# Optimization experiments

Hardware: AMD Instinct MI355X
Metric: run time of the kernel (lower is better)

Reference implementation:

```python
import jax, jax.numpy as jnp
import numpy as np

B, C, H, W = 4, 256, 48, 48
NH = 8
HD = C // NH
SCALE = HD ** -0.5


def setup_inputs() -> dict:
    key = jax.random.key(0)
    ks = jax.random.split(key, 9)
    std = 1.0 / np.sqrt(C)
    return {
        "x": jax.random.normal(ks[0], (B, C, H, W), dtype=jnp.float32),
        "Wq": jax.random.normal(ks[1], (C, C), dtype=jnp.float32) * std,
        "bq": jax.random.normal(ks[2], (C,), dtype=jnp.float32) * std,
        "Wk": jax.random.normal(ks[3], (C, C), dtype=jnp.float32) * std,
        "bk": jax.random.normal(ks[4], (C,), dtype=jnp.float32) * std,
        "Wv": jax.random.normal(ks[5], (C, C), dtype=jnp.float32) * std,
        "bv": jax.random.normal(ks[6], (C,), dtype=jnp.float32) * std,
        "Wo": jax.random.normal(ks[7], (C, C), dtype=jnp.float32) * std,
        "bo": jax.random.normal(ks[8], (C,), dtype=jnp.float32) * std,
    }


def _proj(x, Wm, bm):
    # 1x1 conv == pointwise channel matmul; x: [B,C,H,W], Wm: [out,in]
    return jnp.einsum('bchw,oc->bohw', x, Wm) + bm[None, :, None, None]


def reference(x, Wq, bq, Wk, bk, Wv, bv, Wo, bo):
    b, c, h, w = x.shape
    s = h * w
    # [B,C,H,W] -> [B, NH, S, HD]
    def heads(t):
        return t.reshape(b, NH, HD, s).transpose(0, 1, 3, 2)
    q = heads(_proj(x, Wq, bq))
    k = heads(_proj(x, Wk, bk))
    v = heads(_proj(x, Wv, bv))
    attn = jax.nn.softmax(jnp.einsum('bhsd,bhtd->bhst', q, k) * SCALE, axis=-1)
    out = jnp.einsum('bhst,bhtd->bhsd', attn, v)
    out = out.transpose(0, 1, 3, 2).reshape(b, c, h, w)
    out = _proj(out, Wo, bo)
    return out + x
```

## Files before the change

### kernel.cpp

```cpp
#include <hip/hip_runtime.h>
#include <hip/hip_bf16.h>

#define BATCH 4
#define CCH   256
#define SS    2304
#define NHEAD 8
#define HD    32
#define SCALE_L2E (1.4426950408889634f * 0.17677669529663687f)

using bf16x8 = __attribute__((ext_vector_type(8))) short;
using v4s    = __attribute__((ext_vector_type(4))) short;
using v8s    = __attribute__((ext_vector_type(8))) short;
using f32x4  = __attribute__((ext_vector_type(4))) float;

static __device__ __forceinline__ unsigned short f2bf(float f) {
    union { float f; unsigned u; } a; a.f = f;
    unsigned r = a.u + 0x7fff + ((a.u >> 16) & 1);
    return (unsigned short)(r >> 16);
}
static __device__ __forceinline__ unsigned pk2(float a, float b) {
    return (unsigned)f2bf(a) | ((unsigned)f2bf(b) << 16);
}
static __device__ __forceinline__ v4s pack4(float a, float b, float c, float d) {
    float2 lo; lo.x = a; lo.y = b;
    float2 hi; hi.x = c; hi.y = d;
    union { __hip_bfloat162 h2[2]; v4s s; } u;
    u.h2[0] = __float22bfloat162_rn(lo);
    u.h2[1] = __float22bfloat162_rn(hi);
    return u.s;
}

__global__ __launch_bounds__(256) void prep(const float* __restrict__ Wq, const float* __restrict__ Wk,
                                            const float* __restrict__ Wv, const float* __restrict__ Wo,
                                            const float* __restrict__ x,
                                            unsigned short* __restrict__ wqkv, unsigned short* __restrict__ wo,
                                            unsigned short* __restrict__ xt) {
    __shared__ float T[64][65];
    const int tid = threadIdx.x;
    if (blockIdx.x < 1024) {
        const int idx = blockIdx.x * 256 + tid;
        if (idx < 768 * 256) {
            const int o = idx >> 8, c = idx & 255;
            const float v = (o < 256) ? Wq[idx] : (o < 512) ? Wk[(o - 256) * 256 + c] : Wv[(o - 512) * 256 + c];
            wqkv[idx] = f2bf(v);
        } else {
            const int j = idx - 768 * 256;
            wo[j] = f2bf(Wo[j]);
        }
    } else {
        const int e = blockIdx.x - 1024;
        const int b = e / 144, rem = e % 144;
        const int c0 = (rem / 36) * 64, s0 = (rem % 36) * 64;
        #pragma unroll
        for (int p = 0; p < 16; ++p) {
            const int c = p * 4 + (tid >> 6), s = tid & 63;
            T[c][s] = x[((size_t)(b * CCH + c0 + c)) * SS + s0 + s];
        }
        __syncthreads();
        #pragma unroll
        for (int p = 0; p < 8; ++p) {
            const int s = p * 8 + (tid >> 5), c = (tid & 31) * 2;
            *(unsigned*)&xt[((size_t)(b * SS + s0 + s)) * CCH + c0 + c] = pk2(T[c][s], T[c + 1][s]);
        }
    }
}

__global__ __launch_bounds__(128) void gemm_qkv(const unsigned short* __restrict__ xt,
                                                const unsigned short* __restrict__ wqkv,
                                                const float* __restrict__ bq, const float* __restrict__ bk,
                                                const float* __restrict__ bv,
                                                unsigned short* __restrict__ qt, unsigned short* __restrict__ kt,
                                                unsigned short* __restrict__ vp) {
    __shared__ char Eb[2][9216];
    const int b  = blockIdx.z;
    const int o0 = blockIdx.x * 64, s0 = blockIdx.y * 64;
    const int tid = threadIdx.x, wid = tid >> 6, lane = tid & 63;
    const int lr = lane & 15, lg = lane >> 4;
    const int o_w = o0 + wid * 32, s_w = s0;

    const f32x4 zero4 = {0.f, 0.f, 0.f, 0.f};
    f32x4 acc[2][4];
    #pragma unroll
    for (int ai = 0; ai < 2; ++ai)
        #pragma unroll
        for (int bj = 0; bj < 4; ++bj) acc[ai][bj] = zero4;

    #pragma unroll
    for (int c0 = 0; c0 < 256; c0 += 32) {
        bf16x8 a[2], bb[4];
        #pragma unroll
        for (int ai = 0; ai < 2; ++ai)
            a[ai] = *(const bf16x8*)&wqkv[(size_t)(o_w + ai * 16 + lr) * 256 + c0 + lg * 8];
        #pragma unroll
        for (int bj = 0; bj < 4; ++bj)
            bb[bj] = *(const bf16x8*)&xt[((size_t)b * SS + s_w + bj * 16 + lr) * 256 + c0 + lg * 8];
        #pragma unroll
        for (int ai = 0; ai < 2; ++ai)
            #pragma unroll
            for (int bj = 0; bj < 4; ++bj)
                acc[ai][bj] = __builtin_amdgcn_mfma_f32_16x16x32_bf16(a[ai], bb[bj], acc[ai][bj], 0, 0, 0);
    }

    const int t = o0 >> 8;
    const int o_loc = o_w - t * 256;
    const float* bias = (t == 0) ? bq : (t == 1) ? bk : bv;

    float vals[2][4][4];
    #pragma unroll
    for (int ai = 0; ai < 2; ++ai)
        #pragma unroll
        for (int bj = 0; bj < 4; ++bj)
            #pragma unroll
            for (int i = 0; i < 4; ++i) {
                float vv = acc[ai][bj][i] + bias[o_loc + ai * 16 + 4 * lg + i];
                if (t == 0) vv *= SCALE_L2E;
                vals[ai][bj][i] = vv;
            }

    if (t < 2) {
        unsigned short* dst = (t == 0) ? qt : kt;
        unsigned short* Ls = (unsigned short*)Eb[wid];
        #pragma unroll
        for (int ai = 0; ai < 2; ++ai)
            #pragma unroll
            for (int bj = 0; bj < 4; ++bj) {
                uint2 w;
                w.x = pk2(vals[ai][bj][0], vals[ai][bj][1]);
                w.y = pk2(vals[ai][bj][2], vals[ai][bj][3]);
                *(uint2*)&Ls[(bj * 16 + lr) * 40 + ai * 16 + 4 * lg] = w;
            }
        const int h = o_loc >> 5;
        const size_t base = (size_t)(b * NHEAD + h) * SS;
        #pragma unroll
        for (int p = 0; p < 4; ++p) {
            const int cid = p * 64 + lane;
            const int s_loc = cid >> 2, oc = cid & 3;
            uint4 v = *(const uint4*)&Ls[s_loc * 40 + oc * 8];
            *(uint4*)&dst[(base + s_w + s_loc) * HD + oc * 8] = v;
        }
    } else {
        float* Lf = (float*)Eb[wid];
        #pragma unroll
        for (int ai = 0; ai < 2; ++ai)
            #pragma unroll
            for (int bj = 0; bj < 4; ++bj)
                #pragma unroll
                for (int i = 0; i < 4; ++i)
                    Lf[(ai * 16 + 4 * lg + i) * 68 + bj * 16 + lr] = vals[ai][bj][i];
        #pragma unroll
        for (int p = 0; p < 4; ++p) {
            const int cid = p * 64 + lane;
            const int oc = cid >> 3, sc8 = (cid & 7) * 8;
            float4 f0 = *(const float4*)&Lf[oc * 68 + sc8];
            float4 f1 = *(const float4*)&Lf[oc * 68 + sc8 + 4];
            uint4 w;
            w.x = pk2(f0.x, f0.y); w.y = pk2(f0.z, f0.w);
            w.z = pk2(f1.x, f1.y); w.w = pk2(f1.z, f1.w);
            *(uint4*)&vp[((size_t)(b * CCH) + o_loc + oc) * SS + s_w + sc8] = w;
        }
    }
}


#define SBAR __builtin_amdgcn_sched_barrier(0)

#define STAGE_LOAD(T0) do {                                                                \
    kreg = *(const v8s*)(ksrc + (size_t)(T0) * HD);                                        \
    vl   = *(const v4s*)(vsrc0 + (T0));                                                    \
    vh   = *(const v4s*)(vsrc1 + (T0));                                                    \
} while (0)

#define STAGE_WRITE(BUF) do {                                                              \
    *(v8s*)&Kbuf[BUF][wid * 512 + lane * 8] = kreg;                                        \
    *(v8s*)&Vbuf[BUF][wid * 512 + lane * 8] =                                              \
        __builtin_shufflevector(vl, vh, 0, 1, 2, 3, 4, 5, 6, 7);                           \
} while (0)

#define ATT_COMPUTE(BUF) do {                                                              \
    bf16x8 KF[4]; v8s VV[4];                                                               \
    _Pragma("unroll") for (int tt = 0; tt < 4; ++tt)                                       \
        KF[tt] = *(const bf16x8*)&Kbuf[BUF][tt * 512 + lane * 8];                          \
    _Pragma("unroll") for (int tt = 0; tt < 4; ++tt)                                       \
        VV[tt] = *(const v8s*)&Vbuf[BUF][tt * 512 + lane * 8];                             \
    f32x4 sc[4];                                                                           \
    _Pragma("unroll") for (int tt = 0; tt < 4; ++tt)                                       \
        sc[tt] = __builtin_amdgcn_mfma_f32_16x16x32_bf16(KF[tt], qf, zero4, 0, 0, 0);      \
    float p[16];                                                                           \
    _Pragma("unroll") for (int tt = 0; tt < 4; ++tt)                                       \
        _Pragma("unroll") for (int i = 0; i < 4; ++i)                                      \
            p[tt * 4 + i] = __builtin_amdgcn_exp2f(sc[tt][i]);                             \
    _Pragma("unroll") for (int tt = 0; tt < 4; ++tt)                                       \
        psum += (p[tt * 4] + p[tt * 4 + 1]) + (p[tt * 4 + 2] + p[tt * 4 + 3]);             \
    _Pragma("unroll") for (int tt = 0; tt < 4; ++tt) {                                     \
        const v4s pf = pack4(p[tt * 4], p[tt * 4 + 1], p[tt * 4 + 2], p[tt * 4 + 3]);      \
        const v4s v0 = __builtin_shufflevector(VV[tt], VV[tt], 0, 1, 2, 3);                \
        const v4s v1 = __builtin_shufflevector(VV[tt], VV[tt], 4, 5, 6, 7);                \
        acc[0] = __builtin_amdgcn_mfma_f32_16x16x16bf16_1k(v0, pf, acc[0], 0, 0, 0);       \
        acc[1] = __builtin_amdgcn_mfma_f32_16x16x16bf16_1k(v1, pf, acc[1], 0, 0, 0);       \
    }                                                                                      \
} while (0)

__global__ __launch_bounds__(256, 4) void attn(const unsigned short* __restrict__ qt,
                                               const unsigned short* __restrict__ kt,
                                               const unsigned short* __restrict__ vp,
                                               unsigned short* __restrict__ ot) {
    __shared__ short Kbuf[2][2048];
    __shared__ short Vbuf[2][2048];

    const int tid = threadIdx.x;
    const int wid = tid >> 6, lane = tid & 63;
    const int lr = lane & 15, lg = lane >> 4;

    const int bid = blockIdx.x;
    const int xs = bid & 7, w = bid >> 3;
    const int bh = xs * 4 + w / 36;
    const int q0 = (w % 36) * 64 + wid * 16;
    const int b  = bh >> 3, h = bh & 7;

    const unsigned short* qtb = qt + (size_t)bh * SS * HD;
    const unsigned short* ktb = kt + (size_t)bh * SS * HD;
    const unsigned short* vb  = vp + (size_t)(b * CCH + h * HD) * SS;

    const unsigned short* ksrc  = ktb + (size_t)(wid * 16 + lr) * HD + lg * 8;
    const unsigned short* vsrc0 = vb + (size_t)lr * SS + wid * 16 + lg * 4;
    const unsigned short* vsrc1 = vb + (size_t)(16 + lr) * SS + wid * 16 + lg * 4;

    const f32x4 zero4 = {0.f, 0.f, 0.f, 0.f};

    bf16x8 qf = *(const bf16x8*)&qtb[(size_t)(q0 + lr) * HD + lg * 8];

    f32x4 acc[2];
    acc[0] = zero4; acc[1] = zero4;
    float psum = 0.f;

    v8s kreg; v4s vl, vh;

    STAGE_LOAD(0);
    STAGE_WRITE(0);
    __syncthreads();

    #pragma unroll 1
    for (int ii = 0; ii < 18; ++ii) {
        STAGE_LOAD((2 * ii + 1) * 64);
        SBAR;
        ATT_COMPUTE(0);
        SBAR;
        STAGE_WRITE(1);
        __syncthreads();
        if (ii < 17) {
            STAGE_LOAD((2 * ii + 2) * 64);
        }
        SBAR;
        ATT_COMPUTE(1);
        SBAR;
        if (ii < 17) {
            STAGE_WRITE(0);
        }
        __syncthreads();
    }

    psum += __shfl_xor(psum, 16);
    psum += __shfl_xor(psum, 32);

    const float inv = 1.f / psum;
    #pragma unroll
    for (int dh = 0; dh < 2; ++dh) {
        const float o0v = acc[dh][0] * inv;
        const float o1v = acc[dh][1] * inv;
        const float o2v = acc[dh][2] * inv;
        const float o3v = acc[dh][3] * inv;
        const v4s sv = pack4(o0v, o1v, o2v, o3v);
        *(v4s*)&ot[((size_t)b * SS + q0 + lr) * CCH + h * HD + dh * 16 + 4 * lg] = sv;
    }
}

__global__ __launch_bounds__(128) void gemm_o(const unsigned short* __restrict__ ot,
                                              const unsigned short* __restrict__ wo,
                                              const float* __restrict__ bo, const float* __restrict__ x,
                                              float* __restrict__ out) {
    const int b  = blockIdx.z;
    const int o0 = blockIdx.x * 64, s0 = blockIdx.y * 64;
    const int tid = threadIdx.x, wid = tid >> 6, lane = tid & 63;
    const int lr = lane & 15, lg = lane >> 4;
    const int o_w = o0 + wid * 32, s_w = s0;

    const f32x4 zero4 = {0.f, 0.f, 0.f, 0.f};
    f32x4 acc[2][4];
    #pragma unroll
    for (int ai = 0; ai < 2; ++ai)
        #pragma unroll
        for (int bj = 0; bj < 4; ++bj) acc[ai][bj] = zero4;

    #pragma unroll
    for (int c0 = 0; c0 < 256; c0 += 32) {
        bf16x8 a[2], bb[4];
        #pragma unroll
        for (int ai = 0; ai < 2; ++ai)
            a[ai] = *(const bf16x8*)&wo[(size_t)(o_w + ai * 16 + lr) * 256 + c0 + lg * 8];
        #pragma unroll
        for (int bj = 0; bj < 4; ++bj)
            bb[bj] = *(const bf16x8*)&ot[((size_t)b * SS + s_w + bj * 16 + lr) * 256 + c0 + lg * 8];
        #pragma unroll
        for (int ai = 0; ai < 2; ++ai)
            #pragma unroll
            for (int bj = 0; bj < 4; ++bj)
                acc[ai][bj] = __builtin_amdgcn_mfma_f32_16x16x32_bf16(a[ai], bb[bj], acc[ai][bj], 0, 0, 0);
    }

    #pragma unroll
    for (int ai = 0; ai < 2; ++ai)
        #pragma unroll
        for (int bj = 0; bj < 4; ++bj)
            #pragma unroll
            for (int i = 0; i < 4; ++i) {
                const int o = o_w + ai * 16 + 4 * lg + i;
                const int s = s_w + bj * 16 + lr;
                const size_t idx = (size_t)(b * CCH + o) * SS + s;
                out[idx] = acc[ai][bj][i] + bo[o] + x[idx];
            }
}

extern "C" void kernel_launch(void* const* d_in, const int* in_sizes, int n_in,
                              void* d_out, int out_size, void* d_ws, size_t ws_size,
                              hipStream_t stream) {
    const float* x  = (const float*)d_in[0];
    const float* Wq = (const float*)d_in[1];
    const float* bq = (const float*)d_in[2];
    const float* Wk = (const float*)d_in[3];
    const float* bk = (const float*)d_in[4];
    const float* Wv = (const float*)d_in[5];
    const float* bv = (const float*)d_in[6];
    const float* Wo = (const float*)d_in[7];
    const float* bo = (const float*)d_in[8];
    float* out = (float*)d_out;

    const size_t plane = (size_t)BATCH * CCH * SS;
    unsigned short* xt   = (unsigned short*)d_ws;
    unsigned short* qtw  = xt  + plane;
    unsigned short* ktw  = qtw + plane;
    unsigned short* vpw  = ktw + plane;
    unsigned short* otw  = vpw + plane;
    unsigned short* wqkv = otw + plane;
    unsigned short* wob  = wqkv + 768 * 256;

    prep<<<dim3(1600), dim3(256), 0, stream>>>(Wq, Wk, Wv, Wo, x, wqkv, wob, xt);
    gemm_qkv<<<dim3(12, 36, BATCH), dim3(128), 0, stream>>>(xt, wqkv, bq, bk, bv, qtw, ktw, vpw);
    attn<<<dim3(1152), dim3(256), 0, stream>>>(qtw, ktw, vpw, otw);
    gemm_o<<<dim3(4, 36, BATCH), dim3(128), 0, stream>>>(otw, wob, bo, x, out);
}
```

Baseline: 96.76 us.

## Split attention KV tiles across waves and combine partial sums in LDS

Each wave now handles all 64 queries of the block but only one 16-key slice of every 64-key tile, instead of 16 queries against all 64 keys. Each wave reads only its own slice of K/V from LDS per stage, which cuts LDS read traffic about fourfold. The cost is four times the accumulator registers per wave and a serial three-round reduction through shared memory at the end, with extra barriers and only wave 0 writing the output. Softmax stays max-free, so combining partial sums is exact.

After: 104.9 us. +8.4%, slower.

```diff
diff --git a/kernel.cpp b/kernel.cpp
--- a/kernel.cpp
+++ b/kernel.cpp
@@ -177,26 +177,23 @@
 } while (0)
 
 #define ATT_COMPUTE(BUF) do {                                                              \
-    bf16x8 KF[4]; v8s VV[4];                                                               \
-    _Pragma("unroll") for (int tt = 0; tt < 4; ++tt)                                       \
-        KF[tt] = *(const bf16x8*)&Kbuf[BUF][tt * 512 + lane * 8];                          \
-    _Pragma("unroll") for (int tt = 0; tt < 4; ++tt)                                       \
-        VV[tt] = *(const v8s*)&Vbuf[BUF][tt * 512 + lane * 8];                             \
+    const bf16x8 KF = *(const bf16x8*)&Kbuf[BUF][wid * 512 + lane * 8];                    \
+    const v8s    VV = *(const v8s*)&Vbuf[BUF][wid * 512 + lane * 8];                       \
+    const v4s v0 = __builtin_shufflevector(VV, VV, 0, 1, 2, 3);                            \
+    const v4s v1 = __builtin_shufflevector(VV, VV, 4, 5, 6, 7);                            \
     f32x4 sc[4];                                                                           \
-    _Pragma("unroll") for (int tt = 0; tt < 4; ++tt)                                       \
-        sc[tt] = __builtin_amdgcn_mfma_f32_16x16x32_bf16(KF[tt], qf, zero4, 0, 0, 0);      \
+    _Pragma("unroll") for (int qg = 0; qg < 4; ++qg)                                       \
+        sc[qg] = __builtin_amdgcn_mfma_f32_16x16x32_bf16(KF, qf[qg], zero4, 0, 0, 0);      \
     float p[16];                                                                           \
-    _Pragma("unroll") for (int tt = 0; tt < 4; ++tt)                                       \
+    _Pragma("unroll") for (int qg = 0; qg < 4; ++qg)                                       \
         _Pragma("unroll") for (int i = 0; i < 4; ++i)                                      \
-            p[tt * 4 + i] = __builtin_amdgcn_exp2f(sc[tt][i]);                             \
-    _Pragma("unroll") for (int tt = 0; tt < 4; ++tt)                                       \
-        psum += (p[tt * 4] + p[tt * 4 + 1]) + (p[tt * 4 + 2] + p[tt * 4 + 3]);             \
-    _Pragma("unroll") for (int tt = 0; tt < 4; ++tt) {                                     \
-        const v4s pf = pack4(p[tt * 4], p[tt * 4 + 1], p[tt * 4 + 2], p[tt * 4 + 3]);      \
-        const v4s v0 = __builtin_shufflevector(VV[tt], VV[tt], 0, 1, 2, 3);                \
-        const v4s v1 = __builtin_shufflevector(VV[tt], VV[tt], 4, 5, 6, 7);                \
-        acc[0] = __builtin_amdgcn_mfma_f32_16x16x16bf16_1k(v0, pf, acc[0], 0, 0, 0);       \
-        acc[1] = __builtin_amdgcn_mfma_f32_16x16x16bf16_1k(v1, pf, acc[1], 0, 0, 0);       \
+            p[qg * 4 + i] = __builtin_amdgcn_exp2f(sc[qg][i]);                             \
+    _Pragma("unroll") for (int qg = 0; qg < 4; ++qg)                                       \
+        psum[qg] += (p[qg * 4] + p[qg * 4 + 1]) + (p[qg * 4 + 2] + p[qg * 4 + 3]);         \
+    _Pragma("unroll") for (int qg = 0; qg < 4; ++qg) {                                     \
+        const v4s pf = pack4(p[qg * 4], p[qg * 4 + 1], p[qg * 4 + 2], p[qg * 4 + 3]);      \
+        acc[qg][0] = __builtin_amdgcn_mfma_f32_16x16x16bf16_1k(v0, pf, acc[qg][0], 0, 0, 0); \
+        acc[qg][1] = __builtin_amdgcn_mfma_f32_16x16x16bf16_1k(v1, pf, acc[qg][1], 0, 0, 0); \
     }                                                                                      \
 } while (0)
 
@@ -206,6 +203,7 @@
                                                unsigned short* __restrict__ ot) {
     __shared__ short Kbuf[2][2048];
     __shared__ short Vbuf[2][2048];
+    __shared__ float Cmb[64][37];
 
     const int tid = threadIdx.x;
     const int wid = tid >> 6, lane = tid & 63;
@@ -214,7 +212,7 @@
     const int bid = blockIdx.x;
     const int xs = bid & 7, w = bid >> 3;
     const int bh = xs * 4 + w / 36;
-    const int q0 = (w % 36) * 64 + wid * 16;
+    const int q0 = (w % 36) * 64;
     const int b  = bh >> 3, h = bh & 7;
 
     const unsigned short* qtb = qt + (size_t)bh * SS * HD;
@@ -227,11 +225,15 @@
 
     const f32x4 zero4 = {0.f, 0.f, 0.f, 0.f};
 
-    bf16x8 qf = *(const bf16x8*)&qtb[(size_t)(q0 + lr) * HD + lg * 8];
-
-    f32x4 acc[2];
-    acc[0] = zero4; acc[1] = zero4;
-    float psum = 0.f;
+    bf16x8 qf[4];
+    #pragma unroll
+    for (int qg = 0; qg < 4; ++qg)
+        qf[qg] = *(const bf16x8*)&qtb[(size_t)(q0 + qg * 16 + lr) * HD + lg * 8];
+
+    f32x4 acc[4][2];
+    #pragma unroll
+    for (int qg = 0; qg < 4; ++qg) { acc[qg][0] = zero4; acc[qg][1] = zero4; }
+    float psum[4] = {0.f, 0.f, 0.f, 0.f};
 
     v8s kreg; v4s vl, vh;
 
@@ -259,18 +261,56 @@
         __syncthreads();
     }
 
-    psum += __shfl_xor(psum, 16);
-    psum += __shfl_xor(psum, 32);
-
-    const float inv = 1.f / psum;
-    #pragma unroll
-    for (int dh = 0; dh < 2; ++dh) {
-        const float o0v = acc[dh][0] * inv;
-        const float o1v = acc[dh][1] * inv;
-        const float o2v = acc[dh][2] * inv;
-        const float o3v = acc[dh][3] * inv;
-        const v4s sv = pack4(o0v, o1v, o2v, o3v);
-        *(v4s*)&ot[((size_t)b * SS + q0 + lr) * CCH + h * HD + dh * 16 + 4 * lg] = sv;
+    #pragma unroll
+    for (int qg = 0; qg < 4; ++qg) {
+        psum[qg] += __shfl_xor(psum[qg], 16);
+        psum[qg] += __shfl_xor(psum[qg], 32);
+    }
+
+    #pragma unroll 1
+    for (int r = 1; r < 4; ++r) {
+        __syncthreads();
+        if (wid == r) {
+            float* rec = &Cmb[lane][0];
+            #pragma unroll
+            for (int qg = 0; qg < 4; ++qg) {
+                #pragma unroll
+                for (int dh = 0; dh < 2; ++dh)
+                    #pragma unroll
+                    for (int i = 0; i < 4; ++i)
+                        rec[qg * 8 + dh * 4 + i] = acc[qg][dh][i];
+                rec[32 + qg] = psum[qg];
+            }
+        }
+        __syncthreads();
+        if (wid == 0) {
+            const float* rec = &Cmb[lane][0];
+            #pragma unroll
+            for (int qg = 0; qg < 4; ++qg) {
+                #pragma unroll
+                for (int dh = 0; dh < 2; ++dh)
+                    #pragma unroll
+                    for (int i = 0; i < 4; ++i)
+                        acc[qg][dh][i] += rec[qg * 8 + dh * 4 + i];
+                psum[qg] += rec[32 + qg];
+            }
+        }
+    }
+
+    if (wid == 0) {
+        #pragma unroll
+        for (int qg = 0; qg < 4; ++qg) {
+            const float inv = 1.f / psum[qg];
+            #pragma unroll
+            for (int dh = 0; dh < 2; ++dh) {
+                const float o0v = acc[qg][dh][0] * inv;
+                const float o1v = acc[qg][dh][1] * inv;
+                const float o2v = acc[qg][dh][2] * inv;
+                const float o3v = acc[qg][dh][3] * inv;
+                const v4s sv = pack4(o0v, o1v, o2v, o3v);
+                *(v4s*)&ot[((size_t)b * SS + q0 + qg * 16 + lr) * CCH + h * HD + dh * 16 + 4 * lg] = sv;
+            }
+        }
     }
 }
 
```
